# Performance work log

Measured on AMD Instinct MI355X. Metric: run time of the kernel, lower is better.

Reference implementation:

```python
import jax, jax.numpy as jnp
import numpy as np

NHEAD = 8
DC = 32
IN_CHS = 2 * NHEAD  # cross_coverage and self_coverage both True
EPS = 1e-5  # BatchNorm1d default eps


def conv2d(x, w, pad):
    return jax.lax.conv_general_dilated(
        x, w, window_strides=(1, 1), padding=[(pad, pad), (pad, pad)],
        dimension_numbers=('NCHW', 'OIHW', 'NCHW'))


def setup_inputs() -> dict:
    key = jax.random.key(0)
    ks = jax.random.split(key, 10)
    b, t, H, W = 8, 256, 16, 32
    l = H * W
    prev_attn = jax.random.uniform(ks[0], (b * NHEAD, t, l), dtype=jnp.float32)
    curr_attn = jax.random.uniform(ks[1], (b * NHEAD, t, l), dtype=jnp.float32)
    key_padding_mask = jax.random.uniform(ks[2], (b, l)) < 0.25  # True = padded
    conv_w = jax.random.normal(ks[3], (DC, IN_CHS, 5, 5), jnp.float32) * 0.05
    conv_b = jnp.zeros((DC,), jnp.float32)
    proj_w = jax.random.normal(ks[4], (NHEAD, DC, 1, 1), jnp.float32) * 0.05
    g_w1 = jax.random.normal(ks[5], (IN_CHS // 2, IN_CHS, 3, 3), jnp.float32) * 0.05
    g_b1 = jnp.zeros((IN_CHS // 2,), jnp.float32)
    g_w2 = jax.random.normal(ks[6], (IN_CHS, IN_CHS // 2, 1, 1), jnp.float32) * 0.05
    g_b2 = jnp.zeros((IN_CHS,), jnp.float32)
    bn_gamma = jnp.ones((NHEAD,), jnp.float32)
    bn_beta = jnp.zeros((NHEAD,), jnp.float32)
    return dict(prev_attn=prev_attn, key_padding_mask=key_padding_mask, h=H,
                curr_attn=curr_attn, tgt_vocab=113,
                conv_w=conv_w, conv_b=conv_b, proj_w=proj_w,
                g_w1=g_w1, g_b1=g_b1, g_w2=g_w2, g_b2=g_b2,
                bn_gamma=bn_gamma, bn_beta=bn_beta)


def reference(prev_attn, key_padding_mask, h, curr_attn, tgt_vocab,
              conv_w, conv_b, proj_w, g_w1, g_b1, g_w2, g_b2, bn_gamma, bn_beta):
    n = NHEAD
    b = prev_attn.shape[0] // n
    t = curr_attn.shape[1]
    l = key_padding_mask.shape[1]
    w = l // h

    prev = prev_attn.reshape(b, n, t, l)
    curr = curr_attn.reshape(b, n, t, l)
    attns = jnp.concatenate([prev, curr], axis=1)  # [b, 2n, t, l]
    c = attns.shape[1]

    # gating network on per-step attention images: [(b t), c, h, w]
    attns_bt = attns.transpose(0, 2, 1, 3).reshape(b * t, c, h, w)
    g = jax.nn.relu(conv2d(attns_bt, g_w1, 1) + g_b1[None, :, None, None])
    g = g.mean(axis=(2, 3))  # AdaptiveAvgPool2d((1,1)) -> [(b t), c//2]
    g = jax.nn.sigmoid(jnp.einsum('bi,oi->bo', g, g_w2[:, :, 0, 0]) + g_b2)
    gate = g.reshape(b, t, c).transpose(0, 2, 1)[..., None]  # [b, c, t, 1]

    gated = attns * gate
    cum = jnp.cumsum(gated, axis=2) - gated  # exclusive cumulative coverage
    cum2d = cum.transpose(0, 2, 1, 3).reshape(b * t, c, h, w)

    mask = jnp.broadcast_to(key_padding_mask.reshape(b, 1, 1, h, w),
                            (b, t, 1, h, w)).reshape(b * t, 1, h, w)

    cov = jax.nn.relu(conv2d(cum2d, conv_w, 2) + conv_b[None, :, None, None])
    cov = jnp.where(mask, 0.0, cov)
    cov = jnp.einsum('bdhw,nd->bnhw', cov, proj_w[:, :, 0, 0])  # 1x1 proj, no bias

    # MaskBatchNorm2d: BN statistics over non-masked positions only
    nm = (~mask).astype(cov.dtype)  # [(b t), 1, h, w]
    cnt = nm.sum()
    mean = (cov * nm).sum(axis=(0, 2, 3), keepdims=True) / cnt  # per-channel
    var = (jnp.square(cov - mean) * nm).sum(axis=(0, 2, 3), keepdims=True) / cnt
    xn = (cov - mean) * jax.lax.rsqrt(var + EPS) * bn_gamma[None, :, None, None] \
        + bn_beta[None, :, None, None]
    cov = jnp.where(mask, cov, xn)  # masked positions keep pre-BN values (zeros)

    out = cov.reshape(b, t, n, l).transpose(0, 2, 1, 3).reshape(b * n, t, l)
    return out
```

## Files before the change

kernel.cpp:

```cpp
#include <hip/hip_runtime.h>
#include <hip/hip_bf16.h>

#define BB   8
#define TT   256
#define NH   8
#define CC   16
#define HH   16
#define WW   32
#define LL   512
#define DCH  32
#define GC   8

#define PSC  1928
#define PSG  1736

typedef __attribute__((ext_vector_type(8))) short s8b;
typedef __attribute__((ext_vector_type(4))) float f32x4;

__device__ __forceinline__ ushort f2bfu(float v) {
  __hip_bfloat16 h = __float2bfloat16(v);
  ushort s;
  __builtin_memcpy(&s, &h, 2);
  return s;
}

__global__ __launch_bounds__(256) void k_gen(const float* __restrict__ cw,
                                             const float* __restrict__ pw,
                                             const float* __restrict__ gw1,
                                             ushort* __restrict__ bfrag,
                                             ushort* __restrict__ pwf,
                                             ushort* __restrict__ bfragG,
                                             float* __restrict__ sums) {
  int idx = blockIdx.x * 256 + threadIdx.x;
  if (idx < 17) sums[idx] = 0.f;
  if (idx < 13312) {
    int j = idx & 7, lane = (idx >> 3) & 63, nt = (idx >> 9) & 1, s = idx >> 10;
    int quad = lane >> 4, col = lane & 15;
    int k = s * 32 + quad * 8 + j;
    int n = nt * 16 + col;
    float v = (k < 400) ? cw[(n * CC + (k & 15)) * 25 + (k >> 4)] : 0.f;
    bfrag[idx] = f2bfu(v);
  } else if (idx < 13824) {
    int i2 = idx - 13312;
    int j = i2 & 7, lane = i2 >> 3;
    int quad = lane >> 4, col = lane & 15;
    float v = (col < NH) ? pw[col * DCH + quad * 8 + j] : 0.f;
    pwf[i2] = f2bfu(v);
  } else if (idx < 16384) {
    int i3 = idx - 13824;
    int j = i3 & 7, lane = (i3 >> 3) & 63, s = i3 >> 9;
    int quad = lane >> 4, col = lane & 15;
    int k = s * 32 + quad * 8 + j;
    float v = 0.f;
    if (k < 144 && col < GC) v = gw1[(col * CC + (k & 15)) * 9 + (k >> 4)];
    bfragG[i3] = f2bfu(v);
  }
}

__global__ __launch_bounds__(256, 4) void k_gate(
    const float* __restrict__ prev, const float* __restrict__ curr,
    const ushort* __restrict__ bfragG, const float* __restrict__ gb1,
    const float* __restrict__ gw2, const float* __restrict__ gb2,
    float* __restrict__ gate2) {
  __shared__ __align__(16) ushort img[8 * PSG];
  __shared__ float redg[64];
  __shared__ float pooled[16];

  int tid = threadIdx.x;
  int lane = tid & 63, w = tid >> 6;
  int bt = blockIdx.x;
  int b = bt >> 8, t = bt & 255;
  int quad = lane >> 4, col = lane & 15;
  int qh = quad >> 1, icb = (quad & 1) * 8;

  for (int i = tid; i < PSG; i += 256) ((uint4*)img)[i] = (uint4){0, 0, 0, 0};
  __syncthreads();

#pragma unroll
  for (int it = 0; it < 4; ++it) {
#pragma unroll
    for (int e = 0; e < 2; ++e) {
      int W = ((it * 4 + w) * 2 + e) * 64 + lane;
      int cp = W >> 8, pp = W & 255;
      int l0 = pp * 2;
      const float* src = (cp < 4) ? prev : curr;
      int chb = (cp & 3) * 2;
      const float* p0 = src + ((size_t)(b * NH + chb) * TT + t) * LL + l0;
      float2 fa = *(const float2*)p0;
      float2 fb = *(const float2*)(p0 + TT * LL);
      unsigned lo = (unsigned)f2bfu(fa.x) | ((unsigned)f2bfu(fb.x) << 16);
      unsigned hi = (unsigned)f2bfu(fa.y) | ((unsigned)f2bfu(fb.y) << 16);
      int r = l0 >> 5, x = l0 & 31;
      int slot = (r + 1) * 48 + 8 + x;
      *(uint2*)&img[cp * PSG + slot * 2] = (uint2){lo, hi};
    }
  }
  __syncthreads();

  f32x4 acc[8];
#pragma unroll
  for (int mi = 0; mi < 8; ++mi) acc[mi] = (f32x4){0.f, 0.f, 0.f, 0.f};
  int mtbase = w * 8;
  int ab[8];
#pragma unroll
  for (int mi = 0; mi < 8; ++mi) {
    int mt = mtbase + mi;
    int py = mt >> 1, px = ((mt & 1) << 4) + col;
    ab[mi] = (icb >> 1) * PSG + (py * 48 + 7 + px) * 2;
  }
  const int offE[5] = {0, 2, 49, 96, 98};
  const int offO[5] = {1, 48, 50, 97, 98};
  const s8b* bG = (const s8b*)bfragG;
#pragma unroll
  for (int s = 0; s < 5; ++s) {
    s8b bf = bG[s * 64 + lane];
    int off2 = (qh ? offO[s] : offE[s]) * 2;
#pragma unroll
    for (int mi = 0; mi < 8; ++mi) {
      union { unsigned u[4]; s8b v; } A;
      int a0 = ab[mi] + off2;
#pragma unroll
      for (int p = 0; p < 4; ++p) A.u[p] = *(const unsigned*)&img[a0 + p * PSG];
      acc[mi] = __builtin_amdgcn_mfma_f32_16x16x32_bf16(A.v, bf, acc[mi], 0, 0, 0);
    }
  }

  float gb1c = (col < GC) ? gb1[col] : 0.f;
  float s = 0.f;
#pragma unroll
  for (int mi = 0; mi < 8; ++mi)
#pragma unroll
    for (int r = 0; r < 4; ++r) s += fmaxf(acc[mi][r] + gb1c, 0.f);
  s += __shfl_down(s, 16, 64);
  s += __shfl_down(s, 32, 64);
  if (lane < 16) redg[w * 16 + lane] = s;
  __syncthreads();
  if (tid < 16)
    pooled[tid] = (redg[tid] + redg[16 + tid] + redg[32 + tid] + redg[48 + tid]) *
                  (1.0f / (float)LL);
  __syncthreads();
  if (tid < 16) {
    float z = gb2[tid];
#pragma unroll
    for (int i = 0; i < GC; ++i) z = fmaf(pooled[i], gw2[tid * GC + i], z);
    gate2[(b * CC + tid) * TT + t] = 1.f / (1.f + __expf(-z));
  }
}

__global__ __launch_bounds__(256) void k_cum(const float* __restrict__ prev,
                                             const float* __restrict__ curr,
                                             const float* __restrict__ gate2,
                                             ushort* __restrict__ cum) {
  int idx = blockIdx.x * 256 + threadIdx.x;
  int l = idx & 511;
  int c = (idx >> 9) & 15;
  int b = idx >> 13;
  const float* src = (c < NH) ? prev : curr;
  const float* a = src + (size_t)(b * NH + (c & 7)) * TT * LL + l;
  const float* g = gate2 + (b * CC + c) * TT;
  ushort* o = cum + (size_t)(b * CC + c) * TT * LL + l;
  float run = 0.f;
#pragma unroll 16
  for (int t = 0; t < TT; ++t) {
    float av = a[(size_t)t * LL];
    float gv = g[t];
    o[(size_t)t * LL] = f2bfu(run);
    run = fmaf(av, gv, run);
  }
}

__global__ __launch_bounds__(256, 4) void k_cov(
    const ushort* __restrict__ cum, const ushort* __restrict__ bfrag,
    const ushort* __restrict__ pwf, const float* __restrict__ cb,
    const int* __restrict__ mask, float* __restrict__ out,
    float* __restrict__ sums) {
  __shared__ __align__(16) ushort img[8 * PSC];
  __shared__ __align__(16) ushort scr[4 * 640];
  __shared__ float redp[128];
  __shared__ float redc[4];

  int tid = threadIdx.x;
  int lane = tid & 63, w = tid >> 6;
  int bt = blockIdx.x;
  int b = bt >> 8, t = bt & 255;
  int quad = lane >> 4, col = lane & 15;
  int qh = quad >> 1, icb = (quad & 1) * 8;

  for (int i = tid; i < PSC; i += 256) ((uint4*)img)[i] = (uint4){0, 0, 0, 0};
  __syncthreads();

#pragma unroll
  for (int it = 0; it < 4; ++it) {
#pragma unroll
    for (int e = 0; e < 2; ++e) {
      int W = ((it * 4 + w) * 2 + e) * 64 + lane;
      int cp = W >> 8, pp = W & 255;
      int l0 = pp * 2;
      const ushort* p0 = cum + ((size_t)(b * CC + cp * 2) * TT + t) * LL + l0;
      unsigned a = *(const unsigned*)p0;
      unsigned bb2 = *(const unsigned*)(p0 + TT * LL);
      unsigned lo = (a & 0xFFFFu) | (bb2 << 16);
      unsigned hi = (a >> 16) | (bb2 & 0xFFFF0000u);
      int r = l0 >> 5, x = l0 & 31;
      int slot = (r + 2) * 48 + 8 + x;
      *(uint2*)&img[cp * PSC + slot * 2] = (uint2){lo, hi};
    }
  }
  __syncthreads();

  f32x4 acc[8][2];
#pragma unroll
  for (int mi = 0; mi < 8; ++mi) {
    acc[mi][0] = (f32x4){0.f, 0.f, 0.f, 0.f};
    acc[mi][1] = (f32x4){0.f, 0.f, 0.f, 0.f};
  }
  int mtbase = w * 8;
  int ab[8];
#pragma unroll
  for (int mi = 0; mi < 8; ++mi) {
    int mt = mtbase + mi;
    int py = mt >> 1, px = ((mt & 1) << 4) + col;
    ab[mi] = (icb >> 1) * PSC + (py * 48 + 6 + px) * 2;
  }
  const int offE[13] = {0, 2, 4, 49, 51, 96, 98, 100, 145, 147, 192, 194, 196};
  const int offO[13] = {1, 3, 48, 50, 52, 97, 99, 144, 146, 148, 193, 195, 196};
  const s8b* bfr = (const s8b*)bfrag;
#pragma unroll
  for (int s = 0; s < 13; ++s) {
    s8b bf0 = bfr[(s * 2) * 64 + lane];
    s8b bf1 = bfr[(s * 2 + 1) * 64 + lane];
    int off2 = (qh ? offO[s] : offE[s]) * 2;
#pragma unroll
    for (int mi = 0; mi < 8; ++mi) {
      union { unsigned u[4]; s8b v; } A;
      int a0 = ab[mi] + off2;
#pragma unroll
      for (int p = 0; p < 4; ++p) A.u[p] = *(const unsigned*)&img[a0 + p * PSC];
      acc[mi][0] = __builtin_amdgcn_mfma_f32_16x16x32_bf16(A.v, bf0, acc[mi][0], 0, 0, 0);
      acc[mi][1] = __builtin_amdgcn_mfma_f32_16x16x32_bf16(A.v, bf1, acc[mi][1], 0, 0, 0);
    }
  }

  int wb = w * 640;
  float cb0 = cb[col], cb1 = cb[col + 16];
  s8b pf = ((const s8b*)pwf)[lane];
  float psum = 0.f, psq = 0.f, pcnt = 0.f;
  float* outbase = out + ((size_t)(b * NH + col) * TT + t) * LL;
  const int* mrow = mask + b * LL;
#pragma unroll
  for (int mi = 0; mi < 8; ++mi) {
    int mt = mtbase + mi;
    ushort w0[4], w1[4];
#pragma unroll
    for (int r = 0; r < 4; ++r) {
      w0[r] = f2bfu(fmaxf(acc[mi][0][r] + cb0, 0.f));
      w1[r] = f2bfu(fmaxf(acc[mi][1][r] + cb1, 0.f));
    }
    uint2 pk0, pk1;
    __builtin_memcpy(&pk0, w0, 8);
    __builtin_memcpy(&pk1, w1, 8);
    *(uint2*)&scr[wb + col * 20 + quad * 4] = pk0;
    *(uint2*)&scr[wb + (col + 16) * 20 + quad * 4] = pk1;
    ushort u[8];
#pragma unroll
    for (int e = 0; e < 8; ++e) u[e] = scr[wb + (quad * 8 + e) * 20 + col];
    s8b a2;
    __builtin_memcpy(&a2, u, 16);
    f32x4 zero = {0.f, 0.f, 0.f, 0.f};
    f32x4 d2 = __builtin_amdgcn_mfma_f32_16x16x32_bf16(a2, pf, zero, 0, 0, 0);
    int4 m4 = *(const int4*)(mrow + mt * 16 + quad * 4);
    float k0 = m4.x ? 0.f : 1.f;
    float k1 = m4.y ? 0.f : 1.f;
    float k2 = m4.z ? 0.f : 1.f;
    float k3 = m4.w ? 0.f : 1.f;
    if (col < NH) {
      float* op = outbase + mt * 16 + quad * 4;
      float v0 = d2[0] * k0; op[0] = v0; psum += v0; psq += v0 * v0;
      float v1 = d2[1] * k1; op[1] = v1; psum += v1; psq += v1 * v1;
      float v2 = d2[2] * k2; op[2] = v2; psum += v2; psq += v2 * v2;
      float v3 = d2[3] * k3; op[3] = v3; psum += v3; psq += v3 * v3;
    }
    if (col == 0) pcnt += k0 + k1 + k2 + k3;
  }

  psum += __shfl_down(psum, 16, 64); psum += __shfl_down(psum, 32, 64);
  psq  += __shfl_down(psq, 16, 64);  psq  += __shfl_down(psq, 32, 64);
  pcnt += __shfl_down(pcnt, 16, 64); pcnt += __shfl_down(pcnt, 32, 64);
  if (lane < 16) {
    redp[(w * 16 + lane) * 2] = psum;
    redp[(w * 16 + lane) * 2 + 1] = psq;
    if (lane == 0) redc[w] = pcnt;
  }
  __syncthreads();
  if (tid < 17) {
    float v;
    if (tid < 8) {
      v = redp[tid * 2] + redp[(16 + tid) * 2] + redp[(32 + tid) * 2] + redp[(48 + tid) * 2];
    } else if (tid < 16) {
      int nh = tid - 8;
      v = redp[nh * 2 + 1] + redp[(16 + nh) * 2 + 1] + redp[(32 + nh) * 2 + 1] + redp[(48 + nh) * 2 + 1];
    } else {
      v = redc[0] + redc[1] + redc[2] + redc[3];
    }
    atomicAdd(&sums[tid], v);
  }
}

__global__ __launch_bounds__(256) void k_bn(
    float* __restrict__ out, const float* __restrict__ sums,
    const int* __restrict__ mask, const float* __restrict__ gamma,
    const float* __restrict__ beta) {
  __shared__ float sc[NH], sh[NH];
  int tid = threadIdx.x;
  if (tid < NH) {
    float cnt = sums[16];
    float mean = sums[tid] / cnt;
    float var = sums[NH + tid] / cnt - mean * mean;
    float inv = rsqrtf(var + 1e-5f) * gamma[tid];
    sc[tid] = inv;
    sh[tid] = fmaf(-mean, inv, beta[tid]);
  }
  __syncthreads();
  size_t e = ((size_t)blockIdx.x * 256 + tid) * 8;
  int l = (int)(e & (LL - 1));
  int bn = (int)(e >> 17);
  int n = bn & 7;
  int b = bn >> 3;
  const int4 mv0 = *(const int4*)(mask + b * LL + l);
  const int4 mv1 = *(const int4*)(mask + b * LL + l + 4);
  float4 v0 = *(float4*)(out + e);
  float4 v1 = *(float4*)(out + e + 4);
  float s = sc[n], h = sh[n];
  v0.x = mv0.x ? v0.x : fmaf(v0.x, s, h);
  v0.y = mv0.y ? v0.y : fmaf(v0.y, s, h);
  v0.z = mv0.z ? v0.z : fmaf(v0.z, s, h);
  v0.w = mv0.w ? v0.w : fmaf(v0.w, s, h);
  v1.x = mv1.x ? v1.x : fmaf(v1.x, s, h);
  v1.y = mv1.y ? v1.y : fmaf(v1.y, s, h);
  v1.z = mv1.z ? v1.z : fmaf(v1.z, s, h);
  v1.w = mv1.w ? v1.w : fmaf(v1.w, s, h);
  *(float4*)(out + e) = v0;
  *(float4*)(out + e + 4) = v1;
}

extern "C" void kernel_launch(void* const* d_in, const int* in_sizes, int n_in,
                              void* d_out, int out_size, void* d_ws, size_t ws_size,
                              hipStream_t stream) {
  const float* prev   = (const float*)d_in[0];
  const int*   mask   = (const int*)d_in[1];
  const float* curr   = (const float*)d_in[3];
  const float* conv_w = (const float*)d_in[5];
  const float* conv_b = (const float*)d_in[6];
  const float* proj_w = (const float*)d_in[7];
  const float* g_w1   = (const float*)d_in[8];
  const float* g_b1   = (const float*)d_in[9];
  const float* g_w2   = (const float*)d_in[10];
  const float* g_b2   = (const float*)d_in[11];
  const float* bn_g   = (const float*)d_in[12];
  const float* bn_b   = (const float*)d_in[13];
  float* out = (float*)d_out;

  char* ws = (char*)d_ws;
  ushort* bfrag  = (ushort*)(ws);
  ushort* pwf    = (ushort*)(ws + 26624);
  ushort* bfragG = (ushort*)(ws + 27648);
  float*  sums   = (float*)(ws + 32768);
  float*  gate2  = (float*)(ws + 36864);
  ushort* cum    = (ushort*)(ws + 36864 + 131072);

  k_gen<<<64, 256, 0, stream>>>(conv_w, proj_w, g_w1, bfrag, pwf, bfragG, sums);
  k_gate<<<BB * TT, 256, 0, stream>>>(prev, curr, bfragG, g_b1, g_w2, g_b2, gate2);
  k_cum<<<(BB * CC * LL) / 256, 256, 0, stream>>>(prev, curr, gate2, cum);
  k_cov<<<BB * TT, 256, 0, stream>>>(cum, bfrag, pwf, conv_b, mask, out, sums);
  k_bn<<<(BB * NH * TT * LL) / (256 * 8), 256, 0, stream>>>(out, sums, mask, bn_g, bn_b);
}
```

Before: 200.7 us.

## Repack coverage conv LDS image into 4-channel planes for 64-bit fragment loads

The k_cov shared-memory image changes from 8 planes of channel pairs to 4 planes of 4 interleaved channels, so each MFMA A-fragment is read with two 64-bit LDS loads instead of four 32-bit loads. The staging loop now loads four channels per thread and writes 128-bit words. The gating kernel's staging also widens its global loads to float4 and its LDS stores to uint4. This cuts LDS instruction count in the conv inner loop, at the risk of different bank-conflict patterns and different global-load coalescing.

```diff
diff --git a/kernel.cpp b/kernel.cpp
--- a/kernel.cpp
+++ b/kernel.cpp
@@ -11,7 +11,7 @@
 #define DCH  32
 #define GC   8
 
-#define PSC  1928
+#define PSC4 964
 #define PSG  1736
 
 typedef __attribute__((ext_vector_type(8))) short s8b;
@@ -78,22 +78,21 @@
 
 #pragma unroll
   for (int it = 0; it < 4; ++it) {
-#pragma unroll
-    for (int e = 0; e < 2; ++e) {
-      int W = ((it * 4 + w) * 2 + e) * 64 + lane;
-      int cp = W >> 8, pp = W & 255;
-      int l0 = pp * 2;
-      const float* src = (cp < 4) ? prev : curr;
-      int chb = (cp & 3) * 2;
-      const float* p0 = src + ((size_t)(b * NH + chb) * TT + t) * LL + l0;
-      float2 fa = *(const float2*)p0;
-      float2 fb = *(const float2*)(p0 + TT * LL);
-      unsigned lo = (unsigned)f2bfu(fa.x) | ((unsigned)f2bfu(fb.x) << 16);
-      unsigned hi = (unsigned)f2bfu(fa.y) | ((unsigned)f2bfu(fb.y) << 16);
-      int r = l0 >> 5, x = l0 & 31;
-      int slot = (r + 1) * 48 + 8 + x;
-      *(uint2*)&img[cp * PSG + slot * 2] = (uint2){lo, hi};
-    }
+    int E = it * 256 + tid;
+    int cp = E >> 7, g = E & 127;
+    int l0 = g * 4;
+    const float* src = (cp < 4) ? prev : curr;
+    int chb = (cp & 3) * 2;
+    const float* p0 = src + ((size_t)(b * NH + chb) * TT + t) * LL + l0;
+    float4 f0 = *(const float4*)p0;
+    float4 f1 = *(const float4*)(p0 + (size_t)TT * LL);
+    unsigned w0 = (unsigned)f2bfu(f0.x) | ((unsigned)f2bfu(f1.x) << 16);
+    unsigned w1 = (unsigned)f2bfu(f0.y) | ((unsigned)f2bfu(f1.y) << 16);
+    unsigned w2 = (unsigned)f2bfu(f0.z) | ((unsigned)f2bfu(f1.z) << 16);
+    unsigned w3 = (unsigned)f2bfu(f0.w) | ((unsigned)f2bfu(f1.w) << 16);
+    int r = l0 >> 5, x = l0 & 31;
+    int slot = (r + 1) * 48 + 8 + x;
+    *(uint4*)&img[cp * PSG + slot * 2] = (uint4){w0, w1, w2, w3};
   }
   __syncthreads();
 
@@ -174,7 +173,7 @@
     const ushort* __restrict__ pwf, const float* __restrict__ cb,
     const int* __restrict__ mask, float* __restrict__ out,
     float* __restrict__ sums) {
-  __shared__ __align__(16) ushort img[8 * PSC];
+  __shared__ __align__(16) ushort img[4 * PSC4 * 4];
   __shared__ __align__(16) ushort scr[4 * 640];
   __shared__ float redp[128];
   __shared__ float redc[4];
@@ -184,27 +183,30 @@
   int bt = blockIdx.x;
   int b = bt >> 8, t = bt & 255;
   int quad = lane >> 4, col = lane & 15;
-  int qh = quad >> 1, icb = (quad & 1) * 8;
-
-  for (int i = tid; i < PSC; i += 256) ((uint4*)img)[i] = (uint4){0, 0, 0, 0};
+  int qh = quad >> 1;
+  int p0pl = (quad & 1) * 2;
+
+  for (int i = tid; i < 1928; i += 256) ((uint4*)img)[i] = (uint4){0, 0, 0, 0};
   __syncthreads();
 
 #pragma unroll
   for (int it = 0; it < 4; ++it) {
-#pragma unroll
-    for (int e = 0; e < 2; ++e) {
-      int W = ((it * 4 + w) * 2 + e) * 64 + lane;
-      int cp = W >> 8, pp = W & 255;
-      int l0 = pp * 2;
-      const ushort* p0 = cum + ((size_t)(b * CC + cp * 2) * TT + t) * LL + l0;
-      unsigned a = *(const unsigned*)p0;
-      unsigned bb2 = *(const unsigned*)(p0 + TT * LL);
-      unsigned lo = (a & 0xFFFFu) | (bb2 << 16);
-      unsigned hi = (a >> 16) | (bb2 & 0xFFFF0000u);
-      int r = l0 >> 5, x = l0 & 31;
-      int slot = (r + 2) * 48 + 8 + x;
-      *(uint2*)&img[cp * PSC + slot * 2] = (uint2){lo, hi};
-    }
+    int E = it * 256 + tid;
+    int q = E >> 8;
+    int e = E & 255;
+    int l0 = e * 2;
+    const ushort* p0 = cum + ((size_t)(b * CC + q * 4) * TT + t) * LL + l0;
+    unsigned v0 = *(const unsigned*)p0;
+    unsigned v1 = *(const unsigned*)(p0 + (size_t)TT * LL);
+    unsigned v2 = *(const unsigned*)(p0 + (size_t)2 * TT * LL);
+    unsigned v3 = *(const unsigned*)(p0 + (size_t)3 * TT * LL);
+    unsigned w0 = (v0 & 0xFFFFu) | (v1 << 16);
+    unsigned w1 = (v2 & 0xFFFFu) | (v3 << 16);
+    unsigned w2 = (v0 >> 16) | (v1 & 0xFFFF0000u);
+    unsigned w3 = (v2 >> 16) | (v3 & 0xFFFF0000u);
+    int r = l0 >> 5, x = l0 & 31;
+    int slot = (r + 2) * 48 + 8 + x;
+    *(uint4*)&img[(q * PSC4 + slot) * 4] = (uint4){w0, w1, w2, w3};
   }
   __syncthreads();
 
@@ -220,7 +222,7 @@
   for (int mi = 0; mi < 8; ++mi) {
     int mt = mtbase + mi;
     int py = mt >> 1, px = ((mt & 1) << 4) + col;
-    ab[mi] = (icb >> 1) * PSC + (py * 48 + 6 + px) * 2;
+    ab[mi] = p0pl * PSC4 + py * 48 + 6 + px;
   }
   const int offE[13] = {0, 2, 4, 49, 51, 96, 98, 100, 145, 147, 192, 194, 196};
   const int offO[13] = {1, 3, 48, 50, 52, 97, 99, 144, 146, 148, 193, 195, 196};
@@ -229,13 +231,13 @@
   for (int s = 0; s < 13; ++s) {
     s8b bf0 = bfr[(s * 2) * 64 + lane];
     s8b bf1 = bfr[(s * 2 + 1) * 64 + lane];
-    int off2 = (qh ? offO[s] : offE[s]) * 2;
+    int off = qh ? offO[s] : offE[s];
 #pragma unroll
     for (int mi = 0; mi < 8; ++mi) {
-      union { unsigned u[4]; s8b v; } A;
-      int a0 = ab[mi] + off2;
-#pragma unroll
-      for (int p = 0; p < 4; ++p) A.u[p] = *(const unsigned*)&img[a0 + p * PSC];
+      union { uint2 u2[2]; s8b v; } A;
+      int e0 = ab[mi] + off;
+      A.u2[0] = *(const uint2*)&img[e0 * 4];
+      A.u2[1] = *(const uint2*)&img[(e0 + PSC4) * 4];
       acc[mi][0] = __builtin_amdgcn_mfma_f32_16x16x32_bf16(A.v, bf0, acc[mi][0], 0, 0, 0);
       acc[mi][1] = __builtin_amdgcn_mfma_f32_16x16x32_bf16(A.v, bf1, acc[mi][1], 0, 0, 0);
     }
```

Result: no change. 202.0 us (+0.7%).
